# Optimization experiments

Measured on AMD Instinct MI355X. Metric: run time of the kernel, lower is better.

## Reference

```python
import math
import jax, jax.numpy as jnp
import numpy as np

DIM = 1024
NUM_HEADS = 16
HEAD_DIM = DIM // NUM_HEADS
SCALE = HEAD_DIM ** -0.5
ROPE_BASE = 10000.0


def _rope(x):
    # x: [b, h, t, d]; rotate-half RoPE as in the torch module
    b, h, t, d = x.shape
    half = d // 2
    freqs = jnp.exp(-math.log(ROPE_BASE) * jnp.arange(half, dtype=jnp.float32) / half)
    pos = jnp.arange(t, dtype=jnp.float32)
    angles = pos[:, None] * freqs[None, :]          # [t, half]
    sin = jnp.sin(angles)[None, None, :, :]
    cos = jnp.cos(angles)[None, None, :, :]
    x1, x2 = x[..., :half], x[..., half:]
    return jnp.concatenate([x1 * cos - x2 * sin, x1 * sin + x2 * cos], axis=-1)


def setup_inputs() -> dict:
    key = jax.random.key(0)
    k1, k2, k3, k4 = jax.random.split(key, 4)
    b, t = 2, 2048
    x = jax.random.normal(k1, (b, t, DIM), dtype=jnp.float32)
    # nn.Linear(dim, 3*dim, bias=False): store as [in, out] for x @ W
    w_qkv = jax.random.normal(k2, (DIM, 3 * DIM), dtype=jnp.float32) * (DIM ** -0.5)
    w_proj = jax.random.normal(k3, (DIM, DIM), dtype=jnp.float32) * (DIM ** -0.5)
    b_proj = jax.random.normal(k4, (DIM,), dtype=jnp.float32) * 0.02
    return {"x": x, "w_qkv": w_qkv, "w_proj": w_proj, "b_proj": b_proj}


def reference(x, w_qkv, w_proj, b_proj):
    b, t, c = x.shape
    h, hd = NUM_HEADS, HEAD_DIM
    qkv = (x @ w_qkv).reshape(b, t, 3, h, hd)
    qkv = jnp.transpose(qkv, (2, 0, 3, 1, 4))      # [3, b, h, t, hd]
    q, k, v = qkv[0], qkv[1], qkv[2]
    q, k = _rope(q), _rope(k)
    attn = jnp.einsum('bhqd,bhkd->bhqk', q, k) * SCALE
    causal_mask = jnp.triu(jnp.ones((t, t), dtype=bool), k=1)
    attn = jnp.where(causal_mask[None, None], -jnp.inf, attn)
    attn = jax.nn.softmax(attn, axis=-1)
    out = jnp.einsum('bhqk,bhkd->bhqd', attn, v)
    out = jnp.transpose(out, (0, 2, 1, 3)).reshape(b, t, c)
    return out @ w_proj + b_proj
```

## Files before the change

kernel.cpp:

```cpp
#include <hip/hip_runtime.h>
#include <math.h>

typedef unsigned short u16;
typedef unsigned int u32;
typedef __bf16 bfrag8 __attribute__((ext_vector_type(8)));
typedef float f32x4 __attribute__((ext_vector_type(4)));

#define B_ 2
#define T_ 2048
#define H_ 16
#define D_ 64
#define C_ 1024
#define NQKV_ 3072

#define MFMA_BF16(a, b, c) __builtin_amdgcn_mfma_f32_16x16x32_bf16((a), (b), (c), 0, 0, 0)

__device__ __forceinline__ u16 f2bf(float f) {
  u32 u = __builtin_bit_cast(u32, f);
  u += 0x7fffu + ((u >> 16) & 1u);
  return (u16)(u >> 16);
}

__device__ __forceinline__ void load_lds16(const u16* gp, u16* lp) {
  __builtin_amdgcn_global_load_lds(
      (const __attribute__((address_space(1))) u32*)(const void*)gp,
      (__attribute__((address_space(3))) u32*)(void*)lp, 16, 0, 0);
}

__global__ __launch_bounds__(256) void convert_x(const float* __restrict__ src,
                                                 u16* __restrict__ dst) {
  size_t i = ((size_t)blockIdx.x * 256 + threadIdx.x) * 8;
  const float* s = src + i;
  float4 a = *(const float4*)s, b = *(const float4*)(s + 4);
  union { uint4 v; u16 h[8]; } t;
  t.h[0] = f2bf(a.x); t.h[1] = f2bf(a.y); t.h[2] = f2bf(a.z); t.h[3] = f2bf(a.w);
  t.h[4] = f2bf(b.x); t.h[5] = f2bf(b.y); t.h[6] = f2bf(b.z); t.h[7] = f2bf(b.w);
  *(uint4*)(dst + i) = t.v;
}

__global__ __launch_bounds__(256) void transpose_w(const float* __restrict__ src,
                                                   u16* __restrict__ dst, int K, int N) {
  __shared__ u16 tile[64][65];
  int bx = blockIdx.x * 64;
  int by = blockIdx.y * 64;
  for (int idx = threadIdx.x; idx < 4096; idx += 256) {
    int r = idx >> 6, c = idx & 63;
    tile[r][c] = f2bf(src[(size_t)(by + r) * N + bx + c]);
  }
  __syncthreads();
  for (int idx = threadIdx.x; idx < 4096; idx += 256) {
    int r = idx >> 6, c = idx & 63;
    dst[(size_t)(bx + r) * K + by + c] = tile[c][r];
  }
}

__global__ __launch_bounds__(256) void gemm_qkv_rope(const u16* __restrict__ X,
                                                     const u16* __restrict__ WT,
                                                     u16* __restrict__ qb,
                                                     u16* __restrict__ kb,
                                                     u16* __restrict__ vb) {
  const int K = C_;
  __shared__ __align__(16) u16 As[2][128 * 32];
  __shared__ __align__(16) u16 Bs[2][128 * 32];
  int tid = threadIdx.x;
  int lane = tid & 63, wave = tid >> 6;
  int quad = lane >> 4, lr = lane & 15;
  int m0 = blockIdx.y * 128, n0 = blockIdx.x * 128;
  int wrow = (wave >> 1) * 64, wcol = (wave & 1) * 64;
  int r0 = wave * 32;
  int srow = lane >> 2, skc = (lane & 3) * 8;

  f32x4 zero = {0.f, 0.f, 0.f, 0.f};
  f32x4 acc[4][4];
#pragma unroll
  for (int i = 0; i < 4; i++)
#pragma unroll
    for (int j = 0; j < 4; j++) acc[i][j] = zero;

  const u16* ga0 = X + (size_t)(m0 + r0 + srow) * K + skc;
  const u16* ga1 = X + (size_t)(m0 + r0 + 16 + srow) * K + skc;
  const u16* gb0 = WT + (size_t)(n0 + r0 + srow) * K + skc;
  const u16* gb1 = WT + (size_t)(n0 + r0 + 16 + srow) * K + skc;

  load_lds16(ga0, &As[0][r0 * 32]);
  load_lds16(ga1, &As[0][(r0 + 16) * 32]);
  load_lds16(gb0, &Bs[0][r0 * 32]);
  load_lds16(gb1, &Bs[0][(r0 + 16) * 32]);

  int buf = 0;
  for (int k0 = 0; k0 < K; k0 += 32) {
    __syncthreads();
    if (k0 + 32 < K) {
      load_lds16(ga0 + k0 + 32, &As[buf ^ 1][r0 * 32]);
      load_lds16(ga1 + k0 + 32, &As[buf ^ 1][(r0 + 16) * 32]);
      load_lds16(gb0 + k0 + 32, &Bs[buf ^ 1][r0 * 32]);
      load_lds16(gb1 + k0 + 32, &Bs[buf ^ 1][(r0 + 16) * 32]);
    }
    bfrag8 af[4], bfr[4];
#pragma unroll
    for (int i = 0; i < 4; i++)
      af[i] = *(const bfrag8*)&As[buf][(wrow + i * 16 + lr) * 32 + quad * 8];
#pragma unroll
    for (int j = 0; j < 4; j++)
      bfr[j] = *(const bfrag8*)&Bs[buf][(wcol + j * 16 + lr) * 32 + quad * 8];
#pragma unroll
    for (int i = 0; i < 4; i++)
#pragma unroll
      for (int j = 0; j < 4; j++) acc[i][j] = MFMA_BF16(af[i], bfr[j], acc[i][j]);
    buf ^= 1;
  }

  int colbase = n0 + wcol;
  int which = colbase >> 10;
  int h = (colbase & 1023) >> 6;
  u16* dst = which == 0 ? qb : (which == 1 ? kb : vb);
  float sc0 = (which == 0) ? 0.125f : 1.0f;
  float fr0 = __expf(-0.28782313662425574f * (float)lr);
  float fr1 = __expf(-0.28782313662425574f * (float)(16 + lr));
#pragma unroll
  for (int i = 0; i < 4; i++) {
#pragma unroll
    for (int r = 0; r < 4; r++) {
      int m = m0 + wrow + i * 16 + quad * 4 + r;
      int b = m >> 11, tt = m & 2047;
      size_t base = ((size_t)(b * H_ + h) * T_ + tt) * D_;
      if (which < 2) {
        float sn, cs;
        __sincosf((float)tt * fr0, &sn, &cs);
        dst[base + lr] = f2bf((acc[i][0][r] * cs - acc[i][2][r] * sn) * sc0);
        dst[base + lr + 32] = f2bf((acc[i][0][r] * sn + acc[i][2][r] * cs) * sc0);
        __sincosf((float)tt * fr1, &sn, &cs);
        dst[base + 16 + lr] = f2bf((acc[i][1][r] * cs - acc[i][3][r] * sn) * sc0);
        dst[base + 48 + lr] = f2bf((acc[i][1][r] * sn + acc[i][3][r] * cs) * sc0);
      } else {
#pragma unroll
        for (int j = 0; j < 4; j++) dst[base + j * 16 + lr] = f2bf(acc[i][j][r]);
      }
    }
  }
}

__global__ __launch_bounds__(256) void transpose_v(const u16* __restrict__ v,
                                                   u16* __restrict__ vt) {
  __shared__ u16 tile[64][72];
  int t0 = blockIdx.x * 64;
  int bh = blockIdx.y;
  const u16* src = v + (size_t)bh * T_ * D_;
  u16* dst = vt + (size_t)bh * D_ * T_;
  for (int idx = threadIdx.x; idx < 512; idx += 256) {
    int r = idx >> 3, c8 = (idx & 7) * 8;
    *(uint4*)&tile[r][c8] = *(const uint4*)(src + (size_t)(t0 + r) * D_ + c8);
  }
  __syncthreads();
  for (int idx = threadIdx.x; idx < 512; idx += 256) {
    int d = idx >> 3, t8 = (idx & 7) * 8;
    union { uint4 u; u16 s[8]; } p;
#pragma unroll
    for (int e = 0; e < 8; e++) p.s[e] = tile[t8 + e][d];
    *(uint4*)(dst + (size_t)d * T_ + t0 + t8) = p.u;
  }
}

__global__ __launch_bounds__(256) void attn_k(const u16* __restrict__ qb,
                                              const u16* __restrict__ kb,
                                              const u16* __restrict__ vtb,
                                              u16* __restrict__ ob) {
  __shared__ __align__(16) u16 Ks[2][64 * 64];
  __shared__ __align__(16) u16 Vt[2][64 * 64];
  __shared__ __align__(16) u16 Pst[4][16 * 72];
  int tid = threadIdx.x;
  int lane = tid & 63, wave = tid >> 6;
  int quad = lane >> 4, lr = lane & 15;
  int i = blockIdx.x;
  int bq = 31 - (i >> 5);
  int bh = i & 31;
  int b = bh >> 4, h = bh & 15;
  const u16* Q = qb + (size_t)bh * T_ * D_;
  const u16* Kp = kb + (size_t)bh * T_ * D_;
  const u16* Vp = vtb + (size_t)bh * D_ * T_;
  int qr0 = bq * 64 + wave * 16;
  int r0 = wave * 16;
  int sr = lane >> 3;
  int sc = (((lane & 7) ^ (sr & 7)) * 8);

  int koff0 = ((quad ^ (lr & 7)) << 3);
  int koff1 = (((4 | quad) ^ (lr & 7)) << 3);

  bfrag8 qf[2];
#pragma unroll
  for (int ks = 0; ks < 2; ks++)
    qf[ks] = *(const bfrag8*)(Q + (size_t)(qr0 + lr) * D_ + ks * 32 + quad * 8);

  f32x4 zero = {0.f, 0.f, 0.f, 0.f};
  f32x4 o[4];
#pragma unroll
  for (int nn = 0; nn < 4; nn++) o[nn] = zero;
  float psum = 0.f;

  const u16* gk = Kp + (size_t)(r0 + sr) * D_ + sc;
  const u16* gv = Vp + (size_t)(r0 + sr) * T_ + sc;
  int niter = bq + 1;

  load_lds16(gk, &Ks[0][r0 * 64]);
  load_lds16(gk + (size_t)8 * D_, &Ks[0][(r0 + 8) * 64]);
  load_lds16(gv, &Vt[0][r0 * 64]);
  load_lds16(gv + (size_t)8 * T_, &Vt[0][(r0 + 8) * 64]);

  int buf = 0;
  int qloc = wave * 16 + lr;
  for (int it = 0; it < niter; it++) {
    __syncthreads();
    if (it + 1 < niter) {
      int tkn = (it + 1) * 64;
      load_lds16(gk + (size_t)tkn * D_, &Ks[buf ^ 1][r0 * 64]);
      load_lds16(gk + (size_t)(tkn + 8) * D_, &Ks[buf ^ 1][(r0 + 8) * 64]);
      load_lds16(gv + tkn, &Vt[buf ^ 1][r0 * 64]);
      load_lds16(gv + (size_t)8 * T_ + tkn, &Vt[buf ^ 1][(r0 + 8) * 64]);
    }
    const u16* ks_ = Ks[buf];
    const u16* vt_ = Vt[buf];

    f32x4 s[4];
#pragma unroll
    for (int j = 0; j < 4; j++) s[j] = zero;
#pragma unroll
    for (int j = 0; j < 4; j++) {
      bfrag8 kf0 = *(const bfrag8*)&ks_[(j * 16 + lr) * 64 + koff0];
      bfrag8 kf1 = *(const bfrag8*)&ks_[(j * 16 + lr) * 64 + koff1];
      s[j] = MFMA_BF16(kf0, qf[0], s[j]);
      s[j] = MFMA_BF16(kf1, qf[1], s[j]);
    }

    bool edge = (it == bq);
#pragma unroll
    for (int j = 0; j < 4; j++) {
      float p[4];
#pragma unroll
      for (int r = 0; r < 4; r++) {
        float e = __expf(s[j][r]);
        if (edge) {
          int kvloc = j * 16 + quad * 4 + r;
          e = (kvloc <= qloc) ? e : 0.f;
        }
        p[r] = e;
        psum += e;
      }
      u32 u0 = __builtin_bit_cast(u32, p[0]) + 0x8000u;
      u32 u1 = __builtin_bit_cast(u32, p[1]) + 0x8000u;
      u32 u2 = __builtin_bit_cast(u32, p[2]) + 0x8000u;
      u32 u3 = __builtin_bit_cast(u32, p[3]) + 0x8000u;
      uint2 pk;
      pk.x = (u0 >> 16) | (u1 & 0xffff0000u);
      pk.y = (u2 >> 16) | (u3 & 0xffff0000u);
      *(uint2*)&Pst[wave][lr * 72 + j * 16 + quad * 4] = pk;
    }

#pragma unroll
    for (int ks = 0; ks < 2; ks++) {
      bfrag8 pf = *(const bfrag8*)&Pst[wave][lr * 72 + ks * 32 + quad * 8];
      int ko = ks ? koff1 : koff0;
#pragma unroll
      for (int nn = 0; nn < 4; nn++) {
        bfrag8 vf = *(const bfrag8*)&vt_[(nn * 16 + lr) * 64 + ko];
        o[nn] = MFMA_BF16(pf, vf, o[nn]);
      }
    }
    buf ^= 1;
  }

  float l = psum;
  l += __shfl_xor(l, 16, 64);
  l += __shfl_xor(l, 32, 64);
  float linv = 1.0f / l;

#pragma unroll
  for (int r = 0; r < 4; r++) {
    float lrec = __shfl(linv, quad * 4 + r, 64);
    int row = qr0 + quad * 4 + r;
#pragma unroll
    for (int nn = 0; nn < 4; nn++)
      ob[(size_t)(b * T_ + row) * C_ + h * 64 + nn * 16 + lr] = f2bf(o[nn][r] * lrec);
  }
}

__global__ __launch_bounds__(256) void gemm_proj(const u16* __restrict__ A,
                                                 const u16* __restrict__ WT,
                                                 const float* __restrict__ bias,
                                                 float* __restrict__ out) {
  const int K = C_;
  __shared__ __align__(16) u16 As[2][64 * 32];
  __shared__ __align__(16) u16 Bs[2][128 * 32];
  int tid = threadIdx.x;
  int lane = tid & 63, wave = tid >> 6;
  int quad = lane >> 4, lr = lane & 15;
  int m0 = blockIdx.y * 64, n0 = blockIdx.x * 128;
  int wcol = wave * 32;
  int srow = lane >> 2, skc = (lane & 3) * 8;

  f32x4 zero = {0.f, 0.f, 0.f, 0.f};
  f32x4 acc[4][2];
#pragma unroll
  for (int i = 0; i < 4; i++)
#pragma unroll
    for (int j = 0; j < 2; j++) acc[i][j] = zero;

  const u16* ga = A + (size_t)(m0 + wave * 16 + srow) * K + skc;
  const u16* gb0 = WT + (size_t)(n0 + wave * 32 + srow) * K + skc;
  const u16* gb1 = WT + (size_t)(n0 + wave * 32 + 16 + srow) * K + skc;

  load_lds16(ga, &As[0][wave * 16 * 32]);
  load_lds16(gb0, &Bs[0][wave * 32 * 32]);
  load_lds16(gb1, &Bs[0][(wave * 32 + 16) * 32]);

  int buf = 0;
  for (int k0 = 0; k0 < K; k0 += 32) {
    __syncthreads();
    if (k0 + 32 < K) {
      load_lds16(ga + k0 + 32, &As[buf ^ 1][wave * 16 * 32]);
      load_lds16(gb0 + k0 + 32, &Bs[buf ^ 1][wave * 32 * 32]);
      load_lds16(gb1 + k0 + 32, &Bs[buf ^ 1][(wave * 32 + 16) * 32]);
    }
    bfrag8 af[4], bfr[2];
#pragma unroll
    for (int i = 0; i < 4; i++)
      af[i] = *(const bfrag8*)&As[buf][(i * 16 + lr) * 32 + quad * 8];
#pragma unroll
    for (int j = 0; j < 2; j++)
      bfr[j] = *(const bfrag8*)&Bs[buf][(wcol + j * 16 + lr) * 32 + quad * 8];
#pragma unroll
    for (int i = 0; i < 4; i++)
#pragma unroll
      for (int j = 0; j < 2; j++) acc[i][j] = MFMA_BF16(af[i], bfr[j], acc[i][j]);
    buf ^= 1;
  }

#pragma unroll
  for (int i = 0; i < 4; i++)
#pragma unroll
    for (int r = 0; r < 4; r++) {
      int m = m0 + i * 16 + quad * 4 + r;
#pragma unroll
      for (int j = 0; j < 2; j++) {
        int n = n0 + wcol + j * 16 + lr;
        out[(size_t)m * C_ + n] = acc[i][j][r] + bias[n];
      }
    }
}

extern "C" void kernel_launch(void* const* d_in, const int* in_sizes, int n_in,
                              void* d_out, int out_size, void* d_ws, size_t ws_size,
                              hipStream_t stream) {
  const float* x = (const float*)d_in[0];
  const float* w_qkv = (const float*)d_in[1];
  const float* w_proj = (const float*)d_in[2];
  const float* b_proj = (const float*)d_in[3];

  char* w = (char*)d_ws;
  u16* xb = (u16*)(w + 256);
  u16* vtb = xb;
  u16* regA = xb + (size_t)4096 * 1024;
  u16* wqkvT = regA;
  u16* abuf = regA;
  u16* wprojT = regA + (size_t)4096 * 1024;
  u16* qbuf = wprojT + (size_t)1024 * 1024;
  u16* kbuf = qbuf + (size_t)B_ * H_ * T_ * D_;
  u16* vbuf = kbuf + (size_t)B_ * H_ * T_ * D_;

  convert_x<<<2048, 256, 0, stream>>>(x, xb);
  transpose_w<<<dim3(NQKV_ / 64, C_ / 64), 256, 0, stream>>>(w_qkv, wqkvT, C_, NQKV_);
  transpose_w<<<dim3(C_ / 64, C_ / 64), 256, 0, stream>>>(w_proj, wprojT, C_, C_);
  gemm_qkv_rope<<<dim3(NQKV_ / 128, (B_ * T_) / 128), 256, 0, stream>>>(xb, wqkvT, qbuf, kbuf, vbuf);
  transpose_v<<<dim3(T_ / 64, B_ * H_), 256, 0, stream>>>(vbuf, vtb);
  attn_k<<<1024, 256, 0, stream>>>(qbuf, kbuf, vtb, abuf);
  gemm_proj<<<dim3(C_ / 128, (B_ * T_) / 64), 256, 0, stream>>>(abuf, wprojT, b_proj, (float*)d_out);
}
```

Measured before the change: 192.4 us.

## Fuse prep kernels, register-prefetch QKV GEMM, shrink attention KV tiles with causal skip

Merges the x conversion and both weight transposes into one launch, which removes two kernel launches. The QKV GEMM drops its LDS staging and barriers and instead double-buffers fragments loaded straight from global memory into registers. The attention kernel moves to 32-key tiles with a new swizzle, skips per-wave tiles that lie entirely above the causal diagonal, and reorders query blocks to balance load across CUs. The trade-offs are more register pressure and uncoalesced or repeated global loads in the GEMM, plus twice as many barriers in attention.

```diff
diff --git a/kernel.cpp b/kernel.cpp
--- a/kernel.cpp
+++ b/kernel.cpp
@@ -27,22 +27,36 @@
       (__attribute__((address_space(3))) u32*)(void*)lp, 16, 0, 0);
 }
 
-__global__ __launch_bounds__(256) void convert_x(const float* __restrict__ src,
-                                                 u16* __restrict__ dst) {
-  size_t i = ((size_t)blockIdx.x * 256 + threadIdx.x) * 8;
-  const float* s = src + i;
-  float4 a = *(const float4*)s, b = *(const float4*)(s + 4);
-  union { uint4 v; u16 h[8]; } t;
-  t.h[0] = f2bf(a.x); t.h[1] = f2bf(a.y); t.h[2] = f2bf(a.z); t.h[3] = f2bf(a.w);
-  t.h[4] = f2bf(b.x); t.h[5] = f2bf(b.y); t.h[6] = f2bf(b.z); t.h[7] = f2bf(b.w);
-  *(uint4*)(dst + i) = t.v;
-}
-
-__global__ __launch_bounds__(256) void transpose_w(const float* __restrict__ src,
-                                                   u16* __restrict__ dst, int K, int N) {
+__global__ __launch_bounds__(256) void prep_k(const float* __restrict__ x,
+                                              const float* __restrict__ wqkv,
+                                              const float* __restrict__ wproj,
+                                              u16* __restrict__ xb,
+                                              u16* __restrict__ wqkvT,
+                                              u16* __restrict__ wprojT) {
   __shared__ u16 tile[64][65];
-  int bx = blockIdx.x * 64;
-  int by = blockIdx.y * 64;
+  int bi = blockIdx.x;
+  if (bi < 2048) {
+    size_t i = ((size_t)bi * 256 + threadIdx.x) * 8;
+    const float* s = x + i;
+    float4 a = *(const float4*)s, b = *(const float4*)(s + 4);
+    union { uint4 v; u16 h[8]; } t;
+    t.h[0] = f2bf(a.x); t.h[1] = f2bf(a.y); t.h[2] = f2bf(a.z); t.h[3] = f2bf(a.w);
+    t.h[4] = f2bf(b.x); t.h[5] = f2bf(b.y); t.h[6] = f2bf(b.z); t.h[7] = f2bf(b.w);
+    *(uint4*)(xb + i) = t.v;
+    return;
+  }
+  const float* src;
+  u16* dst;
+  int K, N, bx, by;
+  if (bi < 2816) {
+    int t = bi - 2048;
+    src = wqkv; dst = wqkvT; K = C_; N = NQKV_;
+    bx = (t % 48) * 64; by = (t / 48) * 64;
+  } else {
+    int t = bi - 2816;
+    src = wproj; dst = wprojT; K = C_; N = C_;
+    bx = (t & 15) * 64; by = (t >> 4) * 64;
+  }
   for (int idx = threadIdx.x; idx < 4096; idx += 256) {
     int r = idx >> 6, c = idx & 63;
     tile[r][c] = f2bf(src[(size_t)(by + r) * N + bx + c]);
@@ -60,15 +74,20 @@
                                                      u16* __restrict__ kb,
                                                      u16* __restrict__ vb) {
   const int K = C_;
-  __shared__ __align__(16) u16 As[2][128 * 32];
-  __shared__ __align__(16) u16 Bs[2][128 * 32];
   int tid = threadIdx.x;
   int lane = tid & 63, wave = tid >> 6;
   int quad = lane >> 4, lr = lane & 15;
   int m0 = blockIdx.y * 128, n0 = blockIdx.x * 128;
   int wrow = (wave >> 1) * 64, wcol = (wave & 1) * 64;
-  int r0 = wave * 32;
-  int srow = lane >> 2, skc = (lane & 3) * 8;
+
+  const u16* pa[4];
+  const u16* pb[4];
+#pragma unroll
+  for (int i = 0; i < 4; i++)
+    pa[i] = X + (size_t)(m0 + wrow + i * 16 + lr) * K + quad * 8;
+#pragma unroll
+  for (int j = 0; j < 4; j++)
+    pb[j] = WT + (size_t)(n0 + wcol + j * 16 + lr) * K + quad * 8;
 
   f32x4 zero = {0.f, 0.f, 0.f, 0.f};
   f32x4 acc[4][4];
@@ -77,37 +96,24 @@
 #pragma unroll
     for (int j = 0; j < 4; j++) acc[i][j] = zero;
 
-  const u16* ga0 = X + (size_t)(m0 + r0 + srow) * K + skc;
-  const u16* ga1 = X + (size_t)(m0 + r0 + 16 + srow) * K + skc;
-  const u16* gb0 = WT + (size_t)(n0 + r0 + srow) * K + skc;
-  const u16* gb1 = WT + (size_t)(n0 + r0 + 16 + srow) * K + skc;
-
-  load_lds16(ga0, &As[0][r0 * 32]);
-  load_lds16(ga1, &As[0][(r0 + 16) * 32]);
-  load_lds16(gb0, &Bs[0][r0 * 32]);
-  load_lds16(gb1, &Bs[0][(r0 + 16) * 32]);
-
-  int buf = 0;
+  bfrag8 af[2][4], bf[2][4];
+#pragma unroll
+  for (int i = 0; i < 4; i++) af[0][i] = *(const bfrag8*)(pa[i]);
+#pragma unroll
+  for (int j = 0; j < 4; j++) bf[0][j] = *(const bfrag8*)(pb[j]);
+
   for (int k0 = 0; k0 < K; k0 += 32) {
-    __syncthreads();
+    int cur = (k0 >> 5) & 1, nxt = cur ^ 1;
     if (k0 + 32 < K) {
-      load_lds16(ga0 + k0 + 32, &As[buf ^ 1][r0 * 32]);
-      load_lds16(ga1 + k0 + 32, &As[buf ^ 1][(r0 + 16) * 32]);
-      load_lds16(gb0 + k0 + 32, &Bs[buf ^ 1][r0 * 32]);
-      load_lds16(gb1 + k0 + 32, &Bs[buf ^ 1][(r0 + 16) * 32]);
-    }
-    bfrag8 af[4], bfr[4];
+#pragma unroll
+      for (int i = 0; i < 4; i++) af[nxt][i] = *(const bfrag8*)(pa[i] + k0 + 32);
+#pragma unroll
+      for (int j = 0; j < 4; j++) bf[nxt][j] = *(const bfrag8*)(pb[j] + k0 + 32);
+    }
 #pragma unroll
     for (int i = 0; i < 4; i++)
-      af[i] = *(const bfrag8*)&As[buf][(wrow + i * 16 + lr) * 32 + quad * 8];
-#pragma unroll
-    for (int j = 0; j < 4; j++)
-      bfr[j] = *(const bfrag8*)&Bs[buf][(wcol + j * 16 + lr) * 32 + quad * 8];
-#pragma unroll
-    for (int i = 0; i < 4; i++)
-#pragma unroll
-      for (int j = 0; j < 4; j++) acc[i][j] = MFMA_BF16(af[i], bfr[j], acc[i][j]);
-    buf ^= 1;
+#pragma unroll
+      for (int j = 0; j < 4; j++) acc[i][j] = MFMA_BF16(af[cur][i], bf[cur][j], acc[i][j]);
   }
 
   int colbase = n0 + wcol;
@@ -165,26 +171,32 @@
                                               const u16* __restrict__ kb,
                                               const u16* __restrict__ vtb,
                                               u16* __restrict__ ob) {
-  __shared__ __align__(16) u16 Ks[2][64 * 64];
-  __shared__ __align__(16) u16 Vt[2][64 * 64];
-  __shared__ __align__(16) u16 Pst[4][16 * 72];
+  __shared__ __align__(16) u16 Ks[2][32 * 64];
+  __shared__ __align__(16) u16 Vt[2][64 * 32];
+  __shared__ __align__(16) u16 Pst[4][16 * 40];
   int tid = threadIdx.x;
   int lane = tid & 63, wave = tid >> 6;
   int quad = lane >> 4, lr = lane & 15;
   int i = blockIdx.x;
-  int bq = 31 - (i >> 5);
+  int x = (i >> 5) & 7, qd = i >> 8;
+  int bq = (qd == 0) ? 31 - x : (qd == 1) ? 16 + x : (qd == 2) ? 15 - x : x;
   int bh = i & 31;
   int b = bh >> 4, h = bh & 15;
   const u16* Q = qb + (size_t)bh * T_ * D_;
   const u16* Kp = kb + (size_t)bh * T_ * D_;
   const u16* Vp = vtb + (size_t)bh * D_ * T_;
   int qr0 = bq * 64 + wave * 16;
-  int r0 = wave * 16;
-  int sr = lane >> 3;
-  int sc = (((lane & 7) ^ (sr & 7)) * 8);
+
+  int r0k = wave * 8;
+  int srk = lane >> 3, pk = lane & 7;
+  const u16* gk = Kp + (size_t)(r0k + srk) * D_ + ((pk ^ srk) << 3);
+  int r0v = wave * 16;
+  int srv = lane >> 2, pv = lane & 3;
+  const u16* gv = Vp + (size_t)(r0v + srv) * T_ + (((pv ^ ((srv >> 1) & 3))) << 3);
 
   int koff0 = ((quad ^ (lr & 7)) << 3);
   int koff1 = (((4 | quad) ^ (lr & 7)) << 3);
+  int voff = ((quad ^ ((lr >> 1) & 3)) << 3);
 
   bfrag8 qf[2];
 #pragma unroll
@@ -197,71 +209,61 @@
   for (int nn = 0; nn < 4; nn++) o[nn] = zero;
   float psum = 0.f;
 
-  const u16* gk = Kp + (size_t)(r0 + sr) * D_ + sc;
-  const u16* gv = Vp + (size_t)(r0 + sr) * T_ + sc;
-  int niter = bq + 1;
-
-  load_lds16(gk, &Ks[0][r0 * 64]);
-  load_lds16(gk + (size_t)8 * D_, &Ks[0][(r0 + 8) * 64]);
-  load_lds16(gv, &Vt[0][r0 * 64]);
-  load_lds16(gv + (size_t)8 * T_, &Vt[0][(r0 + 8) * 64]);
+  int niter = 2 * bq + 2;
+  load_lds16(gk, &Ks[0][r0k * 64]);
+  load_lds16(gv, &Vt[0][r0v * 32]);
 
   int buf = 0;
-  int qloc = wave * 16 + lr;
   for (int it = 0; it < niter; it++) {
     __syncthreads();
     if (it + 1 < niter) {
-      int tkn = (it + 1) * 64;
-      load_lds16(gk + (size_t)tkn * D_, &Ks[buf ^ 1][r0 * 64]);
-      load_lds16(gk + (size_t)(tkn + 8) * D_, &Ks[buf ^ 1][(r0 + 8) * 64]);
-      load_lds16(gv + tkn, &Vt[buf ^ 1][r0 * 64]);
-      load_lds16(gv + (size_t)8 * T_ + tkn, &Vt[buf ^ 1][(r0 + 8) * 64]);
-    }
-    const u16* ks_ = Ks[buf];
-    const u16* vt_ = Vt[buf];
-
-    f32x4 s[4];
-#pragma unroll
-    for (int j = 0; j < 4; j++) s[j] = zero;
-#pragma unroll
-    for (int j = 0; j < 4; j++) {
-      bfrag8 kf0 = *(const bfrag8*)&ks_[(j * 16 + lr) * 64 + koff0];
-      bfrag8 kf1 = *(const bfrag8*)&ks_[(j * 16 + lr) * 64 + koff1];
-      s[j] = MFMA_BF16(kf0, qf[0], s[j]);
-      s[j] = MFMA_BF16(kf1, qf[1], s[j]);
-    }
-
-    bool edge = (it == bq);
-#pragma unroll
-    for (int j = 0; j < 4; j++) {
-      float p[4];
-#pragma unroll
-      for (int r = 0; r < 4; r++) {
-        float e = __expf(s[j][r]);
-        if (edge) {
-          int kvloc = j * 16 + quad * 4 + r;
-          e = (kvloc <= qloc) ? e : 0.f;
+      int tkn = (it + 1) * 32;
+      load_lds16(gk + (size_t)tkn * D_, &Ks[buf ^ 1][r0k * 64]);
+      load_lds16(gv + tkn, &Vt[buf ^ 1][r0v * 32]);
+    }
+    int tk = it * 32;
+    if (tk < qr0 + 16) {
+      const u16* ks_ = Ks[buf];
+      const u16* vt_ = Vt[buf];
+
+      f32x4 s[2];
+      s[0] = zero; s[1] = zero;
+#pragma unroll
+      for (int j = 0; j < 2; j++) {
+        bfrag8 kf0 = *(const bfrag8*)&ks_[(j * 16 + lr) * 64 + koff0];
+        bfrag8 kf1 = *(const bfrag8*)&ks_[(j * 16 + lr) * 64 + koff1];
+        s[j] = MFMA_BF16(kf0, qf[0], s[j]);
+        s[j] = MFMA_BF16(kf1, qf[1], s[j]);
+      }
+
+      bool edge = (tk + 32 > qr0);
+#pragma unroll
+      for (int j = 0; j < 2; j++) {
+        float p[4];
+#pragma unroll
+        for (int r = 0; r < 4; r++) {
+          float e = __expf(s[j][r]);
+          if (edge) {
+            int tg = tk + j * 16 + quad * 4 + r;
+            e = (tg <= qr0 + lr) ? e : 0.f;
+          }
+          p[r] = e;
+          psum += e;
         }
-        p[r] = e;
-        psum += e;
-      }
-      u32 u0 = __builtin_bit_cast(u32, p[0]) + 0x8000u;
-      u32 u1 = __builtin_bit_cast(u32, p[1]) + 0x8000u;
-      u32 u2 = __builtin_bit_cast(u32, p[2]) + 0x8000u;
-      u32 u3 = __builtin_bit_cast(u32, p[3]) + 0x8000u;
-      uint2 pk;
-      pk.x = (u0 >> 16) | (u1 & 0xffff0000u);
-      pk.y = (u2 >> 16) | (u3 & 0xffff0000u);
-      *(uint2*)&Pst[wave][lr * 72 + j * 16 + quad * 4] = pk;
-    }
-
-#pragma unroll
-    for (int ks = 0; ks < 2; ks++) {
-      bfrag8 pf = *(const bfrag8*)&Pst[wave][lr * 72 + ks * 32 + quad * 8];
-      int ko = ks ? koff1 : koff0;
+        u32 u0 = __builtin_bit_cast(u32, p[0]) + 0x8000u;
+        u32 u1 = __builtin_bit_cast(u32, p[1]) + 0x8000u;
+        u32 u2 = __builtin_bit_cast(u32, p[2]) + 0x8000u;
+        u32 u3 = __builtin_bit_cast(u32, p[3]) + 0x8000u;
+        uint2 pk2;
+        pk2.x = (u0 >> 16) | (u1 & 0xffff0000u);
+        pk2.y = (u2 >> 16) | (u3 & 0xffff0000u);
+        *(uint2*)&Pst[wave][lr * 40 + j * 16 + quad * 4] = pk2;
+      }
+
+      bfrag8 pf = *(const bfrag8*)&Pst[wave][lr * 40 + quad * 8];
 #pragma unroll
       for (int nn = 0; nn < 4; nn++) {
-        bfrag8 vf = *(const bfrag8*)&vt_[(nn * 16 + lr) * 64 + ko];
+        bfrag8 vf = *(const bfrag8*)&vt_[(nn * 16 + lr) * 32 + voff];
         o[nn] = MFMA_BF16(pf, vf, o[nn]);
       }
     }
@@ -366,9 +368,7 @@
   u16* kbuf = qbuf + (size_t)B_ * H_ * T_ * D_;
   u16* vbuf = kbuf + (size_t)B_ * H_ * T_ * D_;
 
-  convert_x<<<2048, 256, 0, stream>>>(x, xb);
-  transpose_w<<<dim3(NQKV_ / 64, C_ / 64), 256, 0, stream>>>(w_qkv, wqkvT, C_, NQKV_);
-  transpose_w<<<dim3(C_ / 64, C_ / 64), 256, 0, stream>>>(w_proj, wprojT, C_, C_);
+  prep_k<<<3072, 256, 0, stream>>>(x, w_qkv, w_proj, xb, wqkvT, wprojT);
   gemm_qkv_rope<<<dim3(NQKV_ / 128, (B_ * T_) / 128), 256, 0, stream>>>(xb, wqkvT, qbuf, kbuf, vbuf);
   transpose_v<<<dim3(T_ / 64, B_ * H_), 256, 0, stream>>>(vbuf, vtb);
   attn_k<<<1024, 256, 0, stream>>>(qbuf, kbuf, vtb, abuf);
```

Measured after the change: 260.8 us. 1.36x slower.
